# Performance work log

Hardware: AMD Instinct MI355X
Metric: run time of the kernel (lower is better)

The kernel has to match this reference:

```python
import jax, jax.numpy as jnp
import numpy as np

B, T, D = 4096, 64, 256       # expressions, max tokens per expression, encoding dim
N_SYM, N_OCC = 20000, 131072  # symbols, symbol occurrences


def setup_inputs() -> dict:
    key = jax.random.key(0)
    k1, k2, k3, k4, k5 = jax.random.split(key, 5)
    # unique flattened occurrence positions -> deterministic scatter
    rng = np.random.default_rng(0)
    flat_pos = rng.permutation(B * T)[:N_OCC].astype(np.int64)
    return {
        "expressions_encodings": jax.random.normal(k1, (B, T, D), dtype=jnp.float32),
        "symbols_encodings": jax.random.normal(k2, (N_SYM, D), dtype=jnp.float32),
        "Wf": jax.random.normal(k3, (D, 2 * D), dtype=jnp.float32) * 0.05,
        "bf": jnp.zeros((D,), dtype=jnp.float32),
        "Wa": jax.random.normal(k4, (D, 2 * D), dtype=jnp.float32) * 0.05,
        "ba": jnp.zeros((D,), dtype=jnp.float32),
        "expr_idx": jnp.asarray(flat_pos // T),
        "token_idx": jnp.asarray(flat_pos % T),
        "symbol_idx": jax.random.randint(k5, (N_OCC,), 0, N_SYM, dtype=jnp.int64),
    }


def reference(expressions_encodings, symbols_encodings, Wf, bf, Wa, ba,
              expr_idx, token_idx, symbol_idx):
    b, t, d = expressions_encodings.shape
    flat = expressions_encodings.reshape(b * t, d)            # [B*T, D]
    occ_pos = t * expr_idx + token_idx                        # [N_OCC]
    prev = flat[occ_pos]                                      # gather: [N_OCC, D]
    upd = symbols_encodings[symbol_idx]                       # gather: [N_OCC, D]
    concat = jnp.concatenate([prev, upd], axis=-1)            # [N_OCC, 2D]
    forget = jax.nn.sigmoid(concat @ Wf.T + bf)               # forget gate
    add = jax.nn.sigmoid(concat @ Wa.T + ba)                  # add gate
    new_occ = forget * prev + add * upd                       # gated update
    out = flat.at[occ_pos].set(new_occ)                       # scatter back
    return out.reshape(b, t, d)
```

## Files before the change

kernel.cpp:

```cpp
#include <hip/hip_runtime.h>

typedef __attribute__((ext_vector_type(8))) short short8;
typedef __attribute__((ext_vector_type(4))) short short4v;
typedef __attribute__((ext_vector_type(4))) float floatx4;

__device__ __forceinline__ unsigned short f2bf(float f) {
    unsigned int u = __float_as_uint(f);
    u += 0x7FFFu + ((u >> 16) & 1u);
    return (unsigned short)(u >> 16);
}
__device__ __forceinline__ float bf2f(unsigned short s) {
    return __uint_as_float(((unsigned int)s) << 16);
}
__device__ __forceinline__ float sigmoidf(float x) {
    return 1.f / (1.f + __expf(-x));
}

__global__ __launch_bounds__(256)
void convert_w_kernel(const float* __restrict__ Wf,
                      const float* __restrict__ Wa,
                      short* __restrict__ wswz)
{
    int id = blockIdx.x * 256 + threadIdx.x;
    int slot = id & 63;
    int ks   = (id >> 6) & 15;
    int g    = id >> 10;
    int l15  = slot & 15, lk = slot >> 4;
    const float* base = (g < 16) ? (Wf + (long)(g * 16 + l15) * 512)
                                 : (Wa + (long)((g - 16) * 16 + l15) * 512);
    const float* src = base + ks * 32 + lk * 8;
    floatx4 w0 = *(const floatx4*)src;
    floatx4 w1 = *(const floatx4*)(src + 4);
    short8 o;
    o[0] = (short)f2bf(w0[0]); o[1] = (short)f2bf(w0[1]);
    o[2] = (short)f2bf(w0[2]); o[3] = (short)f2bf(w0[3]);
    o[4] = (short)f2bf(w1[0]); o[5] = (short)f2bf(w1[1]);
    o[6] = (short)f2bf(w1[2]); o[7] = (short)f2bf(w1[3]);
    *(short8*)(wswz + (long)id * 8) = o;
}

__global__ __launch_bounds__(256)
void zero_flags_kernel(unsigned int* __restrict__ flags)
{
    flags[blockIdx.x * 256 + threadIdx.x] = 0u;
}

__global__ __launch_bounds__(256)
void mark_kernel(const int* __restrict__ ei, const int* __restrict__ ti,
                 unsigned char* __restrict__ flags, int n)
{
    int i = blockIdx.x * 256 + threadIdx.x;
    if (i < n) flags[64 * ei[i] + ti[i]] = 1;
}

__global__ __launch_bounds__(256)
void copy_rest_kernel(const float* __restrict__ flat,
                      const unsigned char* __restrict__ flags,
                      float* __restrict__ out, int nrows)
{
    const int lane = threadIdx.x & 63;
    const int w0   = (blockIdx.x * 256 + threadIdx.x) >> 6;
    const int nw   = (gridDim.x * 256) >> 6;
    for (int row = w0; row < nrows; row += nw) {
        if (flags[row]) continue;
        const floatx4* s = (const floatx4*)(flat + (long)row * 256);
        floatx4*       o = (floatx4*)(out + (long)row * 256);
        o[lane] = s[lane];
    }
}

__global__ __launch_bounds__(512, 4)
void gate_kernel(const float* __restrict__ flat,
                 const float* __restrict__ syms,
                 const float* __restrict__ bfb,
                 const float* __restrict__ bab,
                 const int* __restrict__ ei,
                 const int* __restrict__ ti,
                 const int* __restrict__ si,
                 const short* __restrict__ wswz,
                 float* __restrict__ out)
{
    __shared__ __align__(16) short A_lds[64 * 512];

    const int tid  = threadIdx.x;
    const int lane = tid & 63;
    const int w    = tid >> 6;
    const int occ0 = blockIdx.x * 64;

    int rowi[8];
    {
        int symi[8];
        #pragma unroll
        for (int i = 0; i < 8; ++i) {
            const int occ = occ0 + w * 8 + i;
            rowi[i] = 64 * ei[occ] + ti[occ];
            symi[i] = si[occ];
        }
        floatx4 va[8], vb[8];
        #pragma unroll
        for (int i = 0; i < 8; ++i) {
            const float* base = (lane < 32)
                ? (flat + (long)rowi[i] * 256 + lane * 8)
                : (syms + (long)symi[i] * 256 + (lane - 32) * 8);
            va[i] = *(const floatx4*)base;
            vb[i] = *(const floatx4*)(base + 4);
        }
        #pragma unroll
        for (int i = 0; i < 8; ++i) {
            short8 o;
            o[0] = (short)f2bf(va[i][0]); o[1] = (short)f2bf(va[i][1]);
            o[2] = (short)f2bf(va[i][2]); o[3] = (short)f2bf(va[i][3]);
            o[4] = (short)f2bf(vb[i][0]); o[5] = (short)f2bf(vb[i][1]);
            o[6] = (short)f2bf(vb[i][2]); o[7] = (short)f2bf(vb[i][3]);
            const int r = w * 8 + i;
            *(short8*)&A_lds[r * 512 + ((lane ^ (r & 7)) << 3)] = o;
        }
    }
    __syncthreads();

    const int l15 = lane & 15;
    const int lk  = lane >> 4;
    const short8* wsv = (const short8*)wswz;

    floatx4 acc[4][4];
    #pragma unroll
    for (int mi = 0; mi < 4; ++mi)
        #pragma unroll
        for (int c = 0; c < 4; ++c)
            acc[mi][c] = (floatx4){0.f, 0.f, 0.f, 0.f};

    #pragma unroll
    for (int ks = 0; ks < 16; ++ks) {
        short8 cb[4];
        #pragma unroll
        for (int mi = 0; mi < 4; ++mi) {
            const int m  = mi * 16 + l15;
            const int ch = (ks * 4 + lk) ^ (m & 7);
            cb[mi] = *(const short8*)&A_lds[m * 512 + (ch << 3)];
        }
        #pragma unroll
        for (int c = 0; c < 4; ++c) {
            const int g = (c < 2) ? (w * 2 + c) : (16 + w * 2 + (c - 2));
            const short8 wf = wsv[(g * 16 + ks) * 64 + lane];
            #pragma unroll
            for (int mi = 0; mi < 4; ++mi)
                acc[mi][c] = __builtin_amdgcn_mfma_f32_16x16x32_bf16(
                    wf, cb[mi], acc[mi][c], 0, 0, 0);
        }
    }
    __syncthreads();

    #pragma unroll
    for (int c = 0; c < 2; ++c) {
        const int d0 = w * 32 + c * 16 + lk * 4;
        const floatx4 bfv = *(const floatx4*)(bfb + d0);
        const floatx4 bav = *(const floatx4*)(bab + d0);
        #pragma unroll
        for (int mi = 0; mi < 4; ++mi) {
            const int m  = mi * 16 + l15;
            const int sw = m & 7;
            const int cp = (d0 >> 3) ^ sw;
            const int cu = (32 + (d0 >> 3)) ^ sw;
            const int sub = d0 & 7;
            short4v pv = *(const short4v*)&A_lds[m * 512 + (cp << 3) + sub];
            short4v uv = *(const short4v*)&A_lds[m * 512 + (cu << 3) + sub];
            short4v o;
            #pragma unroll
            for (int j = 0; j < 4; ++j) {
                float fg = sigmoidf(acc[mi][c][j]     + bfv[j]);
                float ag = sigmoidf(acc[mi][c + 2][j] + bav[j]);
                o[j] = (short)f2bf(fg * bf2f((unsigned short)pv[j])
                                 + ag * bf2f((unsigned short)uv[j]));
            }
            *(short4v*)&A_lds[m * 512 + (cp << 3) + sub] = o;
        }
    }
    __syncthreads();

    #pragma unroll
    for (int i = 0; i < 8; ++i) {
        const int r = w * 8 + i;
        short4v s = *(const short4v*)
            &A_lds[r * 512 + (((lane >> 1) ^ (r & 7)) << 3) + (lane & 1) * 4];
        floatx4 o4;
        o4[0] = bf2f((unsigned short)s[0]);
        o4[1] = bf2f((unsigned short)s[1]);
        o4[2] = bf2f((unsigned short)s[2]);
        o4[3] = bf2f((unsigned short)s[3]);
        *(floatx4*)(out + (long)rowi[i] * 256 + lane * 4) = o4;
    }
}

extern "C" void kernel_launch(void* const* d_in, const int* in_sizes, int n_in,
                              void* d_out, int out_size, void* d_ws, size_t ws_size,
                              hipStream_t stream) {
    const float* flat = (const float*)d_in[0];
    const float* syms = (const float*)d_in[1];
    const float* Wf   = (const float*)d_in[2];
    const float* bf   = (const float*)d_in[3];
    const float* Wa   = (const float*)d_in[4];
    const float* ba   = (const float*)d_in[5];
    const int* ei     = (const int*)d_in[6];
    const int* ti     = (const int*)d_in[7];
    const int* si     = (const int*)d_in[8];
    float* out        = (float*)d_out;

    short* wswz          = (short*)d_ws;
    unsigned char* flags = (unsigned char*)d_ws + 512 * 1024;

    const int n_occ = in_sizes[6];
    const int nrows = out_size / 256;

    zero_flags_kernel<<<nrows / 1024, 256, 0, stream>>>((unsigned int*)flags);
    mark_kernel<<<(n_occ + 255) / 256, 256, 0, stream>>>(ei, ti, flags, n_occ);
    convert_w_kernel<<<128, 256, 0, stream>>>(Wf, Wa, wswz);

    gate_kernel<<<n_occ / 64, 512, 0, stream>>>(flat, syms, bf, ba,
                                                ei, ti, si, wswz, out);

    copy_rest_kernel<<<2048, 256, 0, stream>>>(flat, flags, out, nrows);
}
```

Before: 231.8 us.

## Precompute per-symbol gate logits and software-pipeline occurrence gathers

```diff
diff --git a/kernel.cpp b/kernel.cpp
--- a/kernel.cpp
+++ b/kernel.cpp
@@ -3,6 +3,8 @@
 typedef __attribute__((ext_vector_type(8))) short short8;
 typedef __attribute__((ext_vector_type(4))) short short4v;
 typedef __attribute__((ext_vector_type(4))) float floatx4;
+
+#define NSYM 20000
 
 __device__ __forceinline__ unsigned short f2bf(float f) {
     unsigned int u = __float_as_uint(f);
@@ -15,20 +17,26 @@
 __device__ __forceinline__ float sigmoidf(float x) {
     return 1.f / (1.f + __expf(-x));
 }
+__device__ __forceinline__ short4v pack4(floatx4 v) {
+    short4v o;
+    o[0] = (short)f2bf(v[0]); o[1] = (short)f2bf(v[1]);
+    o[2] = (short)f2bf(v[2]); o[3] = (short)f2bf(v[3]);
+    return o;
+}
 
 __global__ __launch_bounds__(256)
 void convert_w_kernel(const float* __restrict__ Wf,
                       const float* __restrict__ Wa,
-                      short* __restrict__ wswz)
+                      short* __restrict__ wswzP,
+                      short* __restrict__ wswzU)
 {
     int id = blockIdx.x * 256 + threadIdx.x;
-    int slot = id & 63;
-    int ks   = (id >> 6) & 15;
-    int g    = id >> 10;
-    int l15  = slot & 15, lk = slot >> 4;
-    const float* base = (g < 16) ? (Wf + (long)(g * 16 + l15) * 512)
-                                 : (Wa + (long)((g - 16) * 16 + l15) * 512);
-    const float* src = base + ks * 32 + lk * 8;
+    int half = id >> 14;
+    int rem  = id & 16383;
+    int slot = rem & 63, ks = (rem >> 6) & 7, g = rem >> 9;
+    int l15 = slot & 15, lk = slot >> 4;
+    const float* wrow = ((g < 16) ? Wf : Wa) + (long)((g & 15) * 16 + l15) * 512;
+    const float* src  = wrow + half * 256 + ks * 32 + lk * 8;
     floatx4 w0 = *(const floatx4*)src;
     floatx4 w1 = *(const floatx4*)(src + 4);
     short8 o;
@@ -36,7 +44,8 @@
     o[2] = (short)f2bf(w0[2]); o[3] = (short)f2bf(w0[3]);
     o[4] = (short)f2bf(w1[0]); o[5] = (short)f2bf(w1[1]);
     o[6] = (short)f2bf(w1[2]); o[7] = (short)f2bf(w1[3]);
-    *(short8*)(wswz + (long)id * 8) = o;
+    short* dst = half ? wswzU : wswzP;
+    *(short8*)(dst + (long)((g * 8 + ks) * 64 + slot) * 8) = o;
 }
 
 __global__ __launch_bounds__(256)
@@ -70,124 +79,206 @@
 }
 
 __global__ __launch_bounds__(512, 4)
-void gate_kernel(const float* __restrict__ flat,
+void syms_logits_kernel(const float* __restrict__ syms,
+                        const float* __restrict__ bfb,
+                        const float* __restrict__ bab,
+                        const short* __restrict__ wswzU,
+                        short* __restrict__ symLg)
+{
+    __shared__ __align__(16) short S_lds[64 * 256];
+    const int tid = threadIdx.x;
+    const int r0  = blockIdx.x * 64;
+    {
+        const int r = tid >> 3, se = tid & 7;
+        const int s = min(r0 + r, NSYM - 1);
+        const float* srow = syms + (long)s * 256;
+        #pragma unroll
+        for (int i = 0; i < 8; ++i) {
+            const int gi = i * 8 + se;
+            floatx4 v = *(const floatx4*)(srow + gi * 4);
+            const int cb = gi >> 1, hf = gi & 1;
+            *(short4v*)&S_lds[r * 256 + ((cb ^ (r & 7)) << 3) + hf * 4] = pack4(v);
+        }
+    }
+    __syncthreads();
+
+    const int lane = tid & 63, w = tid >> 6, l15 = lane & 15, lk = lane >> 4;
+    floatx4 acc[4][4];
+    #pragma unroll
+    for (int mi = 0; mi < 4; ++mi)
+        #pragma unroll
+        for (int c = 0; c < 4; ++c)
+            acc[mi][c] = (floatx4){0.f, 0.f, 0.f, 0.f};
+
+    const short8* wsv = (const short8*)wswzU;
+    #pragma unroll
+    for (int ks = 0; ks < 8; ++ks) {
+        short8 cb[4];
+        #pragma unroll
+        for (int mi = 0; mi < 4; ++mi) {
+            const int m  = mi * 16 + l15;
+            const int ch = (ks * 4 + lk) ^ (m & 7);
+            cb[mi] = *(const short8*)&S_lds[m * 256 + (ch << 3)];
+        }
+        #pragma unroll
+        for (int c = 0; c < 4; ++c) {
+            const int g = (c < 2) ? (w * 2 + c) : (16 + w * 2 + (c - 2));
+            const short8 wf = wsv[(g * 8 + ks) * 64 + lane];
+            #pragma unroll
+            for (int mi = 0; mi < 4; ++mi)
+                acc[mi][c] = __builtin_amdgcn_mfma_f32_16x16x32_bf16(
+                    wf, cb[mi], acc[mi][c], 0, 0, 0);
+        }
+    }
+
+    #pragma unroll
+    for (int c = 0; c < 2; ++c) {
+        const int d0 = w * 32 + c * 16 + lk * 4;
+        const floatx4 bF = *(const floatx4*)(bfb + d0);
+        const floatx4 bA = *(const floatx4*)(bab + d0);
+        #pragma unroll
+        for (int mi = 0; mi < 4; ++mi) {
+            const int m = mi * 16 + l15;
+            const int s = r0 + m;
+            if (s < NSYM) {
+                short4v oF, oA;
+                #pragma unroll
+                for (int j = 0; j < 4; ++j) {
+                    oF[j] = (short)f2bf(acc[mi][c][j]     + bF[j]);
+                    oA[j] = (short)f2bf(acc[mi][c + 2][j] + bA[j]);
+                }
+                *(short4v*)(symLg + (long)s * 512 + d0)       = oF;
+                *(short4v*)(symLg + (long)s * 512 + 256 + d0) = oA;
+            }
+        }
+    }
+}
+
+__global__ __launch_bounds__(512, 4)
+void main_kernel(const float* __restrict__ flat,
                  const float* __restrict__ syms,
-                 const float* __restrict__ bfb,
-                 const float* __restrict__ bab,
                  const int* __restrict__ ei,
                  const int* __restrict__ ti,
                  const int* __restrict__ si,
-                 const short* __restrict__ wswz,
+                 const short* __restrict__ wswzP,
+                 const short* __restrict__ symLg,
                  float* __restrict__ out)
 {
-    __shared__ __align__(16) short A_lds[64 * 512];
+    __shared__ __align__(16) short L[32768];
 
     const int tid  = threadIdx.x;
-    const int lane = tid & 63;
-    const int w    = tid >> 6;
-    const int occ0 = blockIdx.x * 64;
-
-    int rowi[8];
-    {
-        int symi[8];
-        #pragma unroll
-        for (int i = 0; i < 8; ++i) {
-            const int occ = occ0 + w * 8 + i;
-            rowi[i] = 64 * ei[occ] + ti[occ];
-            symi[i] = si[occ];
-        }
-        floatx4 va[8], vb[8];
-        #pragma unroll
-        for (int i = 0; i < 8; ++i) {
-            const float* base = (lane < 32)
-                ? (flat + (long)rowi[i] * 256 + lane * 8)
-                : (syms + (long)symi[i] * 256 + (lane - 32) * 8);
-            va[i] = *(const floatx4*)base;
-            vb[i] = *(const floatx4*)(base + 4);
-        }
-        #pragma unroll
-        for (int i = 0; i < 8; ++i) {
-            short8 o;
-            o[0] = (short)f2bf(va[i][0]); o[1] = (short)f2bf(va[i][1]);
-            o[2] = (short)f2bf(va[i][2]); o[3] = (short)f2bf(va[i][3]);
-            o[4] = (short)f2bf(vb[i][0]); o[5] = (short)f2bf(vb[i][1]);
-            o[6] = (short)f2bf(vb[i][2]); o[7] = (short)f2bf(vb[i][3]);
-            const int r = w * 8 + i;
-            *(short8*)&A_lds[r * 512 + ((lane ^ (r & 7)) << 3)] = o;
-        }
-    }
-    __syncthreads();
-
-    const int l15 = lane & 15;
-    const int lk  = lane >> 4;
-    const short8* wsv = (const short8*)wswz;
-
-    floatx4 acc[4][4];
+    const int lane = tid & 63, w = tid >> 6, l15 = lane & 15, lk = lane >> 4;
+    const int r = tid >> 4, se = tid & 15;
+    const int base_occ = blockIdx.x * 256;
+
+    floatx4 pv[4], uv[4];
+    short8  sl[4];
+    auto issue = [&](int occ0) {
+        const int occ = occ0 + r;
+        const long rowp = 64 * ei[occ] + ti[occ];
+        const long syr  = si[occ];
+        const float* pr = flat + rowp * 256;
+        const float* ur = syms + syr * 256;
+        const short* lr = symLg + syr * 512;
+        #pragma unroll
+        for (int i = 0; i < 4; ++i) {
+            const int gi = i * 16 + se;
+            pv[i] = *(const floatx4*)(pr + gi * 4);
+            uv[i] = *(const floatx4*)(ur + gi * 4);
+            sl[i] = *(const short8*)(lr + gi * 8);
+        }
+    };
+
+    issue(base_occ);
+
+    const short8* wsv = (const short8*)wswzP;
+
     #pragma unroll
-    for (int mi = 0; mi < 4; ++mi)
-        #pragma unroll
-        for (int c = 0; c < 4; ++c)
-            acc[mi][c] = (floatx4){0.f, 0.f, 0.f, 0.f};
-
-    #pragma unroll
-    for (int ks = 0; ks < 16; ++ks) {
-        short8 cb[4];
-        #pragma unroll
-        for (int mi = 0; mi < 4; ++mi) {
-            const int m  = mi * 16 + l15;
-            const int ch = (ks * 4 + lk) ^ (m & 7);
-            cb[mi] = *(const short8*)&A_lds[m * 512 + (ch << 3)];
-        }
-        #pragma unroll
-        for (int c = 0; c < 4; ++c) {
-            const int g = (c < 2) ? (w * 2 + c) : (16 + w * 2 + (c - 2));
-            const short8 wf = wsv[(g * 16 + ks) * 64 + lane];
-            #pragma unroll
-            for (int mi = 0; mi < 4; ++mi)
-                acc[mi][c] = __builtin_amdgcn_mfma_f32_16x16x32_bf16(
-                    wf, cb[mi], acc[mi][c], 0, 0, 0);
-        }
-    }
-    __syncthreads();
-
-    #pragma unroll
-    for (int c = 0; c < 2; ++c) {
-        const int d0 = w * 32 + c * 16 + lk * 4;
-        const floatx4 bfv = *(const floatx4*)(bfb + d0);
-        const floatx4 bav = *(const floatx4*)(bab + d0);
-        #pragma unroll
-        for (int mi = 0; mi < 4; ++mi) {
-            const int m  = mi * 16 + l15;
-            const int sw = m & 7;
-            const int cp = (d0 >> 3) ^ sw;
-            const int cu = (32 + (d0 >> 3)) ^ sw;
-            const int sub = d0 & 7;
-            short4v pv = *(const short4v*)&A_lds[m * 512 + (cp << 3) + sub];
-            short4v uv = *(const short4v*)&A_lds[m * 512 + (cu << 3) + sub];
-            short4v o;
-            #pragma unroll
-            for (int j = 0; j < 4; ++j) {
-                float fg = sigmoidf(acc[mi][c][j]     + bfv[j]);
-                float ag = sigmoidf(acc[mi][c + 2][j] + bav[j]);
-                o[j] = (short)f2bf(fg * bf2f((unsigned short)pv[j])
-                                 + ag * bf2f((unsigned short)uv[j]));
+    for (int t = 0; t < 8; ++t) {
+        const int occ0 = base_occ + t * 32;
+        if (t) __syncthreads();
+        #pragma unroll
+        for (int i = 0; i < 4; ++i) {
+            const int gi = i * 16 + se;
+            const int cb = gi >> 1, hf = gi & 1;
+            const int so = ((cb ^ (r & 7)) << 3) + hf * 4;
+            *(short4v*)&L[r * 256 + so]        = pack4(pv[i]);
+            *(short4v*)&L[8192 + r * 256 + so] = pack4(uv[i]);
+            *(short8*)&L[16384 + r * 512 + ((gi ^ (r & 7)) << 3)] = sl[i];
+        }
+        __syncthreads();
+
+        if (t < 7) issue(occ0 + 32);
+
+        floatx4 acc[2][4];
+        #pragma unroll
+        for (int mi = 0; mi < 2; ++mi)
+            #pragma unroll
+            for (int c = 0; c < 4; ++c)
+                acc[mi][c] = (floatx4){0.f, 0.f, 0.f, 0.f};
+
+        #pragma unroll
+        for (int ks = 0; ks < 8; ++ks) {
+            short8 cb2[2];
+            #pragma unroll
+            for (int mi = 0; mi < 2; ++mi) {
+                const int m  = mi * 16 + l15;
+                const int ch = (ks * 4 + lk) ^ (m & 7);
+                cb2[mi] = *(const short8*)&L[m * 256 + (ch << 3)];
             }
-            *(short4v*)&A_lds[m * 512 + (cp << 3) + sub] = o;
-        }
-    }
-    __syncthreads();
-
-    #pragma unroll
-    for (int i = 0; i < 8; ++i) {
-        const int r = w * 8 + i;
-        short4v s = *(const short4v*)
-            &A_lds[r * 512 + (((lane >> 1) ^ (r & 7)) << 3) + (lane & 1) * 4];
-        floatx4 o4;
-        o4[0] = bf2f((unsigned short)s[0]);
-        o4[1] = bf2f((unsigned short)s[1]);
-        o4[2] = bf2f((unsigned short)s[2]);
-        o4[3] = bf2f((unsigned short)s[3]);
-        *(floatx4*)(out + (long)rowi[i] * 256 + lane * 4) = o4;
+            #pragma unroll
+            for (int c = 0; c < 4; ++c) {
+                const int g = (c < 2) ? (2 * w + c) : (16 + 2 * w + (c - 2));
+                const short8 wf = wsv[(g * 8 + ks) * 64 + lane];
+                acc[0][c] = __builtin_amdgcn_mfma_f32_16x16x32_bf16(
+                    wf, cb2[0], acc[0][c], 0, 0, 0);
+                acc[1][c] = __builtin_amdgcn_mfma_f32_16x16x32_bf16(
+                    wf, cb2[1], acc[1][c], 0, 0, 0);
+            }
+        }
+        __syncthreads();
+
+        #pragma unroll
+        for (int cc = 0; cc < 2; ++cc) {
+            const int d0  = (2 * w + cc) * 16 + lk * 4;
+            const int pch = d0 >> 3;
+            const int ps  = d0 & 7;
+            #pragma unroll
+            for (int mi = 0; mi < 2; ++mi) {
+                const int m = mi * 16 + l15, sw = m & 7;
+                const int slot = ((pch ^ sw) << 3) + ps;
+                short4v pvv = *(const short4v*)&L[m * 256 + slot];
+                short4v uvv = *(const short4v*)&L[8192 + m * 256 + slot];
+                short4v sF  = *(const short4v*)&L[16384 + m * 512 + slot];
+                short4v sA  = *(const short4v*)&L[16384 + m * 512 +
+                                                  (((32 + pch) ^ sw) << 3) + ps];
+                short4v o;
+                #pragma unroll
+                for (int j = 0; j < 4; ++j) {
+                    float fg = sigmoidf(acc[mi][cc][j]     + bf2f((unsigned short)sF[j]));
+                    float ag = sigmoidf(acc[mi][2 + cc][j] + bf2f((unsigned short)sA[j]));
+                    o[j] = (short)f2bf(fg * bf2f((unsigned short)pvv[j])
+                                     + ag * bf2f((unsigned short)uvv[j]));
+                }
+                *(short4v*)&L[m * 256 + slot] = o;
+            }
+        }
+        __syncthreads();
+
+        #pragma unroll
+        for (int i = 0; i < 4; ++i) {
+            const int rr  = w * 4 + i;
+            const int occ = occ0 + rr;
+            const long orow = 64 * ei[occ] + ti[occ];
+            short4v sv = *(const short4v*)
+                &L[rr * 256 + (((lane >> 1) ^ (rr & 7)) << 3) + (lane & 1) * 4];
+            floatx4 o4;
+            o4[0] = bf2f((unsigned short)sv[0]);
+            o4[1] = bf2f((unsigned short)sv[1]);
+            o4[2] = bf2f((unsigned short)sv[2]);
+            o4[3] = bf2f((unsigned short)sv[3]);
+            *(floatx4*)(out + orow * 256 + lane * 4) = o4;
+        }
     }
 }
 
@@ -205,18 +296,22 @@
     const int* si     = (const int*)d_in[8];
     float* out        = (float*)d_out;
 
-    short* wswz          = (short*)d_ws;
-    unsigned char* flags = (unsigned char*)d_ws + 512 * 1024;
+    short* wswzP         = (short*)d_ws;
+    short* wswzU         = (short*)d_ws + 131072;
+    unsigned char* flags = (unsigned char*)d_ws + 524288;
+    short* symLg         = (short*)((char*)d_ws + 786432);
 
     const int n_occ = in_sizes[6];
     const int nrows = out_size / 256;
 
     zero_flags_kernel<<<nrows / 1024, 256, 0, stream>>>((unsigned int*)flags);
     mark_kernel<<<(n_occ + 255) / 256, 256, 0, stream>>>(ei, ti, flags, n_occ);
-    convert_w_kernel<<<128, 256, 0, stream>>>(Wf, Wa, wswz);
-
-    gate_kernel<<<n_occ / 64, 512, 0, stream>>>(flat, syms, bf, ba,
-                                                ei, ti, si, wswz, out);
+    convert_w_kernel<<<128, 256, 0, stream>>>(Wf, Wa, wswzP, wswzU);
+    syms_logits_kernel<<<(NSYM + 63) / 64, 512, 0, stream>>>(syms, bf, ba,
+                                                             wswzU, symLg);
+
+    main_kernel<<<n_occ / 256, 512, 0, stream>>>(flat, syms, ei, ti, si,
+                                                 wswzP, symLg, out);
 
     copy_rest_kernel<<<2048, 256, 0, stream>>>(flat, flags, out, nrows);
 }
```

Result: slower. 295.1 us (+27.3%).

## Stream all rows in dense tiles with inverse symbol map instead of gather+copy

Applied to the files above, without the earlier changes.

```diff
diff --git a/kernel.cpp b/kernel.cpp
--- a/kernel.cpp
+++ b/kernel.cpp
@@ -2,6 +2,7 @@
 
 typedef __attribute__((ext_vector_type(8))) short short8;
 typedef __attribute__((ext_vector_type(4))) short short4v;
+typedef __attribute__((ext_vector_type(2))) unsigned int uint2v;
 typedef __attribute__((ext_vector_type(4))) float floatx4;
 
 __device__ __forceinline__ unsigned short f2bf(float f) {
@@ -14,6 +15,13 @@
 }
 __device__ __forceinline__ float sigmoidf(float x) {
     return 1.f / (1.f + __expf(-x));
+}
+__device__ __forceinline__ short4v pack4(floatx4 v) {
+    unsigned int a, b;
+    asm("v_cvt_pk_bf16_f32 %0, %1, %2" : "=v"(a) : "v"(v[0]), "v"(v[1]));
+    asm("v_cvt_pk_bf16_f32 %0, %1, %2" : "=v"(b) : "v"(v[2]), "v"(v[3]));
+    uint2v u; u[0] = a; u[1] = b;
+    return __builtin_bit_cast(short4v, u);
 }
 
 __global__ __launch_bounds__(256)
@@ -40,154 +48,165 @@
 }
 
 __global__ __launch_bounds__(256)
-void zero_flags_kernel(unsigned int* __restrict__ flags)
-{
-    flags[blockIdx.x * 256 + threadIdx.x] = 0u;
+void zero_inv_kernel(int* __restrict__ inv)
+{
+    inv[blockIdx.x * 256 + threadIdx.x] = 0;
 }
 
 __global__ __launch_bounds__(256)
-void mark_kernel(const int* __restrict__ ei, const int* __restrict__ ti,
-                 unsigned char* __restrict__ flags, int n)
+void scatter_inv_kernel(const int* __restrict__ ei, const int* __restrict__ ti,
+                        const int* __restrict__ si, int* __restrict__ inv, int n)
 {
     int i = blockIdx.x * 256 + threadIdx.x;
-    if (i < n) flags[64 * ei[i] + ti[i]] = 1;
-}
-
-__global__ __launch_bounds__(256)
-void copy_rest_kernel(const float* __restrict__ flat,
-                      const unsigned char* __restrict__ flags,
-                      float* __restrict__ out, int nrows)
-{
-    const int lane = threadIdx.x & 63;
-    const int w0   = (blockIdx.x * 256 + threadIdx.x) >> 6;
-    const int nw   = (gridDim.x * 256) >> 6;
-    for (int row = w0; row < nrows; row += nw) {
-        if (flags[row]) continue;
-        const floatx4* s = (const floatx4*)(flat + (long)row * 256);
-        floatx4*       o = (floatx4*)(out + (long)row * 256);
-        o[lane] = s[lane];
-    }
+    if (i < n) inv[64 * ei[i] + ti[i]] = si[i] + 1;
 }
 
 __global__ __launch_bounds__(512, 4)
-void gate_kernel(const float* __restrict__ flat,
-                 const float* __restrict__ syms,
-                 const float* __restrict__ bfb,
-                 const float* __restrict__ bab,
-                 const int* __restrict__ ei,
-                 const int* __restrict__ ti,
-                 const int* __restrict__ si,
-                 const short* __restrict__ wswz,
-                 float* __restrict__ out)
-{
-    __shared__ __align__(16) short A_lds[64 * 512];
+void stream_kernel(const float* __restrict__ flat,
+                   const float* __restrict__ syms,
+                   const float* __restrict__ bfb,
+                   const float* __restrict__ bab,
+                   const int* __restrict__ inv,
+                   const short* __restrict__ wswz,
+                   float* __restrict__ out, int tiles_per_block)
+{
+    __shared__ __align__(16) short P[64 * 256];
+    __shared__ __align__(16) short U[64 * 256];
+    __shared__ int flg[64];
 
     const int tid  = threadIdx.x;
-    const int lane = tid & 63;
-    const int w    = tid >> 6;
-    const int occ0 = blockIdx.x * 64;
-
-    int rowi[8];
-    {
-        int symi[8];
+    const int lane = tid & 63, w = tid >> 6, l15 = lane & 15, lk = lane >> 4;
+    const int tt0  = blockIdx.x * tiles_per_block;
+
+    floatx4 pv[8];
+    auto issueP = [&](int tile) {
+        const float* src = flat + (long)tile * 16384 + tid * 4;
+        #pragma unroll
+        for (int i = 0; i < 8; ++i) pv[i] = *(const floatx4*)(src + i * 2048);
+    };
+    issueP(tt0);
+
+    const short8* wsv = (const short8*)wswz;
+
+    for (int t = 0; t < tiles_per_block; ++t) {
+        const int tile = tt0 + t;
+        const int row0 = tile * 64;
+        if (t) __syncthreads();
+
+        if (tid < 64) flg[tid] = inv[row0 + tid];
+
+        const int r16 = tid >> 4, se = tid & 15;
+        const int symA = inv[row0 + r16];
+        const int symB = inv[row0 + 32 + r16];
+        floatx4 uva[4], uvb[4];
+        if (symA > 0) {
+            const float* ur = syms + (long)(symA - 1) * 256;
+            #pragma unroll
+            for (int i = 0; i < 4; ++i)
+                uva[i] = *(const floatx4*)(ur + (i * 16 + se) * 4);
+        }
+        if (symB > 0) {
+            const float* ur = syms + (long)(symB - 1) * 256;
+            #pragma unroll
+            for (int i = 0; i < 4; ++i)
+                uvb[i] = *(const floatx4*)(ur + (i * 16 + se) * 4);
+        }
+
         #pragma unroll
         for (int i = 0; i < 8; ++i) {
-            const int occ = occ0 + w * 8 + i;
-            rowi[i] = 64 * ei[occ] + ti[occ];
-            symi[i] = si[occ];
-        }
-        floatx4 va[8], vb[8];
+            const int f  = tid + i * 512;
+            const int rr = f >> 6;
+            const int gi = f & 63;
+            const int cb = gi >> 1, hf = gi & 1;
+            *(short4v*)&P[rr * 256 + ((cb ^ (rr & 7)) << 3) + hf * 4] = pack4(pv[i]);
+        }
+        if (symA > 0) {
+            #pragma unroll
+            for (int i = 0; i < 4; ++i) {
+                const int gi = i * 16 + se, cb = gi >> 1, hf = gi & 1;
+                *(short4v*)&U[r16 * 256 + ((cb ^ (r16 & 7)) << 3) + hf * 4] = pack4(uva[i]);
+            }
+        }
+        if (symB > 0) {
+            const int rr = 32 + r16;
+            #pragma unroll
+            for (int i = 0; i < 4; ++i) {
+                const int gi = i * 16 + se, cb = gi >> 1, hf = gi & 1;
+                *(short4v*)&U[rr * 256 + ((cb ^ (rr & 7)) << 3) + hf * 4] = pack4(uvb[i]);
+            }
+        }
+        __syncthreads();
+
+        if (t + 1 < tiles_per_block) issueP(tile + 1);
+
+        floatx4 acc[4][4];
+        #pragma unroll
+        for (int mi = 0; mi < 4; ++mi)
+            #pragma unroll
+            for (int c = 0; c < 4; ++c)
+                acc[mi][c] = (floatx4){0.f, 0.f, 0.f, 0.f};
+
+        #pragma unroll
+        for (int ks = 0; ks < 16; ++ks) {
+            short8 cb2[4];
+            #pragma unroll
+            for (int mi = 0; mi < 4; ++mi) {
+                const int m = mi * 16 + l15;
+                cb2[mi] = (ks < 8)
+                    ? *(const short8*)&P[m * 256 + (((ks * 4 + lk) ^ (m & 7)) << 3)]
+                    : *(const short8*)&U[m * 256 + ((((ks - 8) * 4 + lk) ^ (m & 7)) << 3)];
+            }
+            #pragma unroll
+            for (int c = 0; c < 4; ++c) {
+                const int g = (c < 2) ? (w * 2 + c) : (16 + w * 2 + (c - 2));
+                const short8 wf = wsv[(g * 16 + ks) * 64 + lane];
+                #pragma unroll
+                for (int mi = 0; mi < 4; ++mi)
+                    acc[mi][c] = __builtin_amdgcn_mfma_f32_16x16x32_bf16(
+                        wf, cb2[mi], acc[mi][c], 0, 0, 0);
+            }
+        }
+        __syncthreads();
+
+        #pragma unroll
+        for (int c = 0; c < 2; ++c) {
+            const int d0 = w * 32 + c * 16 + lk * 4;
+            const floatx4 bfv = *(const floatx4*)(bfb + d0);
+            const floatx4 bav = *(const floatx4*)(bab + d0);
+            #pragma unroll
+            for (int mi = 0; mi < 4; ++mi) {
+                const int m = mi * 16 + l15;
+                if (flg[m] > 0) {
+                    const int sw = m & 7;
+                    const int slot = (((d0 >> 3) ^ sw) << 3) + (d0 & 7);
+                    short4v pvv = *(const short4v*)&P[m * 256 + slot];
+                    short4v uvv = *(const short4v*)&U[m * 256 + slot];
+                    floatx4 res;
+                    #pragma unroll
+                    for (int j = 0; j < 4; ++j) {
+                        float fg = sigmoidf(acc[mi][c][j]     + bfv[j]);
+                        float ag = sigmoidf(acc[mi][c + 2][j] + bav[j]);
+                        res[j] = fg * bf2f((unsigned short)pvv[j])
+                               + ag * bf2f((unsigned short)uvv[j]);
+                    }
+                    *(short4v*)&P[m * 256 + slot] = pack4(res);
+                }
+            }
+        }
+        __syncthreads();
+
         #pragma unroll
         for (int i = 0; i < 8; ++i) {
-            const float* base = (lane < 32)
-                ? (flat + (long)rowi[i] * 256 + lane * 8)
-                : (syms + (long)symi[i] * 256 + (lane - 32) * 8);
-            va[i] = *(const floatx4*)base;
-            vb[i] = *(const floatx4*)(base + 4);
-        }
-        #pragma unroll
-        for (int i = 0; i < 8; ++i) {
-            short8 o;
-            o[0] = (short)f2bf(va[i][0]); o[1] = (short)f2bf(va[i][1]);
-            o[2] = (short)f2bf(va[i][2]); o[3] = (short)f2bf(va[i][3]);
-            o[4] = (short)f2bf(vb[i][0]); o[5] = (short)f2bf(vb[i][1]);
-            o[6] = (short)f2bf(vb[i][2]); o[7] = (short)f2bf(vb[i][3]);
-            const int r = w * 8 + i;
-            *(short8*)&A_lds[r * 512 + ((lane ^ (r & 7)) << 3)] = o;
-        }
-    }
-    __syncthreads();
-
-    const int l15 = lane & 15;
-    const int lk  = lane >> 4;
-    const short8* wsv = (const short8*)wswz;
-
-    floatx4 acc[4][4];
-    #pragma unroll
-    for (int mi = 0; mi < 4; ++mi)
-        #pragma unroll
-        for (int c = 0; c < 4; ++c)
-            acc[mi][c] = (floatx4){0.f, 0.f, 0.f, 0.f};
-
-    #pragma unroll
-    for (int ks = 0; ks < 16; ++ks) {
-        short8 cb[4];
-        #pragma unroll
-        for (int mi = 0; mi < 4; ++mi) {
-            const int m  = mi * 16 + l15;
-            const int ch = (ks * 4 + lk) ^ (m & 7);
-            cb[mi] = *(const short8*)&A_lds[m * 512 + (ch << 3)];
-        }
-        #pragma unroll
-        for (int c = 0; c < 4; ++c) {
-            const int g = (c < 2) ? (w * 2 + c) : (16 + w * 2 + (c - 2));
-            const short8 wf = wsv[(g * 16 + ks) * 64 + lane];
-            #pragma unroll
-            for (int mi = 0; mi < 4; ++mi)
-                acc[mi][c] = __builtin_amdgcn_mfma_f32_16x16x32_bf16(
-                    wf, cb[mi], acc[mi][c], 0, 0, 0);
-        }
-    }
-    __syncthreads();
-
-    #pragma unroll
-    for (int c = 0; c < 2; ++c) {
-        const int d0 = w * 32 + c * 16 + lk * 4;
-        const floatx4 bfv = *(const floatx4*)(bfb + d0);
-        const floatx4 bav = *(const floatx4*)(bab + d0);
-        #pragma unroll
-        for (int mi = 0; mi < 4; ++mi) {
-            const int m  = mi * 16 + l15;
-            const int sw = m & 7;
-            const int cp = (d0 >> 3) ^ sw;
-            const int cu = (32 + (d0 >> 3)) ^ sw;
-            const int sub = d0 & 7;
-            short4v pv = *(const short4v*)&A_lds[m * 512 + (cp << 3) + sub];
-            short4v uv = *(const short4v*)&A_lds[m * 512 + (cu << 3) + sub];
-            short4v o;
-            #pragma unroll
-            for (int j = 0; j < 4; ++j) {
-                float fg = sigmoidf(acc[mi][c][j]     + bfv[j]);
-                float ag = sigmoidf(acc[mi][c + 2][j] + bav[j]);
-                o[j] = (short)f2bf(fg * bf2f((unsigned short)pv[j])
-                                 + ag * bf2f((unsigned short)uv[j]));
-            }
-            *(short4v*)&A_lds[m * 512 + (cp << 3) + sub] = o;
-        }
-    }
-    __syncthreads();
-
-    #pragma unroll
-    for (int i = 0; i < 8; ++i) {
-        const int r = w * 8 + i;
-        short4v s = *(const short4v*)
-            &A_lds[r * 512 + (((lane >> 1) ^ (r & 7)) << 3) + (lane & 1) * 4];
-        floatx4 o4;
-        o4[0] = bf2f((unsigned short)s[0]);
-        o4[1] = bf2f((unsigned short)s[1]);
-        o4[2] = bf2f((unsigned short)s[2]);
-        o4[3] = bf2f((unsigned short)s[3]);
-        *(floatx4*)(out + (long)rowi[i] * 256 + lane * 4) = o4;
+            const int rr = w * 8 + i;
+            short4v s = *(const short4v*)
+                &P[rr * 256 + (((lane >> 1) ^ (rr & 7)) << 3) + (lane & 1) * 4];
+            floatx4 o4;
+            o4[0] = bf2f((unsigned short)s[0]);
+            o4[1] = bf2f((unsigned short)s[1]);
+            o4[2] = bf2f((unsigned short)s[2]);
+            o4[3] = bf2f((unsigned short)s[3]);
+            *(floatx4*)(out + (long)(row0 + rr) * 256 + lane * 4) = o4;
+        }
     }
 }
 
@@ -205,18 +224,20 @@
     const int* si     = (const int*)d_in[8];
     float* out        = (float*)d_out;
 
-    short* wswz          = (short*)d_ws;
-    unsigned char* flags = (unsigned char*)d_ws + 512 * 1024;
+    short* wswz = (short*)d_ws;
+    int*   inv  = (int*)((char*)d_ws + 512 * 1024);
 
     const int n_occ = in_sizes[6];
     const int nrows = out_size / 256;
 
-    zero_flags_kernel<<<nrows / 1024, 256, 0, stream>>>((unsigned int*)flags);
-    mark_kernel<<<(n_occ + 255) / 256, 256, 0, stream>>>(ei, ti, flags, n_occ);
+    zero_inv_kernel<<<nrows / 256, 256, 0, stream>>>(inv);
+    scatter_inv_kernel<<<(n_occ + 255) / 256, 256, 0, stream>>>(ei, ti, si,
+                                                                inv, n_occ);
     convert_w_kernel<<<128, 256, 0, stream>>>(Wf, Wa, wswz);
 
-    gate_kernel<<<n_occ / 64, 512, 0, stream>>>(flat, syms, bf, ba,
-                                                ei, ti, si, wswz, out);
-
-    copy_rest_kernel<<<2048, 256, 0, stream>>>(flat, flags, out, nrows);
-}
+    const int ntiles = nrows / 64;
+    const int nblk   = 512;
+    const int tpb    = ntiles / nblk;
+    stream_kernel<<<nblk, 512, 0, stream>>>(flat, syms, bf, ba, inv, wswz,
+                                            out, tpb);
+}
```

Measured after the change: 806.7 us. 248% more time.

## Split gate GEMM into symbol and prev halves to overlap gather latency

Applied to the files above, without the earlier changes.

```diff
diff --git a/kernel.cpp b/kernel.cpp
--- a/kernel.cpp
+++ b/kernel.cpp
@@ -2,6 +2,7 @@
 
 typedef __attribute__((ext_vector_type(8))) short short8;
 typedef __attribute__((ext_vector_type(4))) short short4v;
+typedef __attribute__((ext_vector_type(2))) unsigned int uint2v;
 typedef __attribute__((ext_vector_type(4))) float floatx4;
 
 __device__ __forceinline__ unsigned short f2bf(float f) {
@@ -14,6 +15,13 @@
 }
 __device__ __forceinline__ float sigmoidf(float x) {
     return 1.f / (1.f + __expf(-x));
+}
+__device__ __forceinline__ short4v pack4(floatx4 v) {
+    unsigned int a, b;
+    asm("v_cvt_pk_bf16_f32 %0, %1, %2" : "=v"(a) : "v"(v[0]), "v"(v[1]));
+    asm("v_cvt_pk_bf16_f32 %0, %1, %2" : "=v"(b) : "v"(v[2]), "v"(v[3]));
+    uint2v u; u[0] = a; u[1] = b;
+    return __builtin_bit_cast(short4v, u);
 }
 
 __global__ __launch_bounds__(256)
@@ -80,47 +88,40 @@
                  const short* __restrict__ wswz,
                  float* __restrict__ out)
 {
-    __shared__ __align__(16) short A_lds[64 * 512];
+    __shared__ __align__(16) short P[64 * 256];
+    __shared__ __align__(16) short U[64 * 256];
 
     const int tid  = threadIdx.x;
     const int lane = tid & 63;
     const int w    = tid >> 6;
     const int occ0 = blockIdx.x * 64;
-
-    int rowi[8];
-    {
-        int symi[8];
-        #pragma unroll
-        for (int i = 0; i < 8; ++i) {
-            const int occ = occ0 + w * 8 + i;
-            rowi[i] = 64 * ei[occ] + ti[occ];
-            symi[i] = si[occ];
-        }
-        floatx4 va[8], vb[8];
-        #pragma unroll
-        for (int i = 0; i < 8; ++i) {
-            const float* base = (lane < 32)
-                ? (flat + (long)rowi[i] * 256 + lane * 8)
-                : (syms + (long)symi[i] * 256 + (lane - 32) * 8);
-            va[i] = *(const floatx4*)base;
-            vb[i] = *(const floatx4*)(base + 4);
-        }
-        #pragma unroll
-        for (int i = 0; i < 8; ++i) {
-            short8 o;
-            o[0] = (short)f2bf(va[i][0]); o[1] = (short)f2bf(va[i][1]);
-            o[2] = (short)f2bf(va[i][2]); o[3] = (short)f2bf(va[i][3]);
-            o[4] = (short)f2bf(vb[i][0]); o[5] = (short)f2bf(vb[i][1]);
-            o[6] = (short)f2bf(vb[i][2]); o[7] = (short)f2bf(vb[i][3]);
-            const int r = w * 8 + i;
-            *(short8*)&A_lds[r * 512 + ((lane ^ (r & 7)) << 3)] = o;
-        }
-    }
-    __syncthreads();
-
-    const int l15 = lane & 15;
-    const int lk  = lane >> 4;
-    const short8* wsv = (const short8*)wswz;
+    const int l15  = lane & 15;
+    const int lk   = lane >> 4;
+
+    int rowi[8], symi[8];
+    #pragma unroll
+    for (int i = 0; i < 8; ++i) {
+        const int occ = occ0 + w * 8 + i;
+        rowi[i] = 64 * ei[occ] + ti[occ];
+        symi[i] = si[occ];
+    }
+
+    floatx4 uv[8];
+    #pragma unroll
+    for (int i = 0; i < 8; ++i)
+        uv[i] = *(const floatx4*)(syms + (long)symi[i] * 256 + lane * 4);
+    floatx4 pv[8];
+    #pragma unroll
+    for (int i = 0; i < 8; ++i)
+        pv[i] = *(const floatx4*)(flat + (long)rowi[i] * 256 + lane * 4);
+
+    const int cb = lane >> 1, hf = lane & 1;
+    #pragma unroll
+    for (int i = 0; i < 8; ++i) {
+        const int r = w * 8 + i;
+        *(short4v*)&U[r * 256 + ((cb ^ (r & 7)) << 3) + hf * 4] = pack4(uv[i]);
+    }
+    __syncthreads();
 
     floatx4 acc[4][4];
     #pragma unroll
@@ -129,14 +130,46 @@
         for (int c = 0; c < 4; ++c)
             acc[mi][c] = (floatx4){0.f, 0.f, 0.f, 0.f};
 
-    #pragma unroll
-    for (int ks = 0; ks < 16; ++ks) {
-        short8 cb[4];
+    const short8* wsv = (const short8*)wswz;
+
+    __builtin_amdgcn_s_setprio(1);
+    #pragma unroll
+    for (int ks = 0; ks < 8; ++ks) {
+        short8 cb2[4];
         #pragma unroll
         for (int mi = 0; mi < 4; ++mi) {
             const int m  = mi * 16 + l15;
             const int ch = (ks * 4 + lk) ^ (m & 7);
-            cb[mi] = *(const short8*)&A_lds[m * 512 + (ch << 3)];
+            cb2[mi] = *(const short8*)&U[m * 256 + (ch << 3)];
+        }
+        #pragma unroll
+        for (int c = 0; c < 4; ++c) {
+            const int g = (c < 2) ? (w * 2 + c) : (16 + w * 2 + (c - 2));
+            const short8 wf = wsv[(g * 16 + 8 + ks) * 64 + lane];
+            #pragma unroll
+            for (int mi = 0; mi < 4; ++mi)
+                acc[mi][c] = __builtin_amdgcn_mfma_f32_16x16x32_bf16(
+                    wf, cb2[mi], acc[mi][c], 0, 0, 0);
+        }
+    }
+    __builtin_amdgcn_s_setprio(0);
+
+    #pragma unroll
+    for (int i = 0; i < 8; ++i) {
+        const int r = w * 8 + i;
+        *(short4v*)&P[r * 256 + ((cb ^ (r & 7)) << 3) + hf * 4] = pack4(pv[i]);
+    }
+    __syncthreads();
+
+    __builtin_amdgcn_s_setprio(1);
+    #pragma unroll
+    for (int ks = 0; ks < 8; ++ks) {
+        short8 cb2[4];
+        #pragma unroll
+        for (int mi = 0; mi < 4; ++mi) {
+            const int m  = mi * 16 + l15;
+            const int ch = (ks * 4 + lk) ^ (m & 7);
+            cb2[mi] = *(const short8*)&P[m * 256 + (ch << 3)];
         }
         #pragma unroll
         for (int c = 0; c < 4; ++c) {
@@ -145,9 +178,10 @@
             #pragma unroll
             for (int mi = 0; mi < 4; ++mi)
                 acc[mi][c] = __builtin_amdgcn_mfma_f32_16x16x32_bf16(
-                    wf, cb[mi], acc[mi][c], 0, 0, 0);
-        }
-    }
+                    wf, cb2[mi], acc[mi][c], 0, 0, 0);
+        }
+    }
+    __builtin_amdgcn_s_setprio(0);
     __syncthreads();
 
     #pragma unroll
@@ -159,29 +193,27 @@
         for (int mi = 0; mi < 4; ++mi) {
             const int m  = mi * 16 + l15;
             const int sw = m & 7;
-            const int cp = (d0 >> 3) ^ sw;
-            const int cu = (32 + (d0 >> 3)) ^ sw;
-            const int sub = d0 & 7;
-            short4v pv = *(const short4v*)&A_lds[m * 512 + (cp << 3) + sub];
-            short4v uv = *(const short4v*)&A_lds[m * 512 + (cu << 3) + sub];
-            short4v o;
+            const int slot = (((d0 >> 3) ^ sw) << 3) + (d0 & 7);
+            short4v pvv = *(const short4v*)&P[m * 256 + slot];
+            short4v uvv = *(const short4v*)&U[m * 256 + slot];
+            floatx4 res;
             #pragma unroll
             for (int j = 0; j < 4; ++j) {
                 float fg = sigmoidf(acc[mi][c][j]     + bfv[j]);
                 float ag = sigmoidf(acc[mi][c + 2][j] + bav[j]);
-                o[j] = (short)f2bf(fg * bf2f((unsigned short)pv[j])
-                                 + ag * bf2f((unsigned short)uv[j]));
+                res[j] = fg * bf2f((unsigned short)pvv[j])
+                       + ag * bf2f((unsigned short)uvv[j]);
             }
-            *(short4v*)&A_lds[m * 512 + (cp << 3) + sub] = o;
-        }
-    }
-    __syncthreads();
-
-    #pragma unroll
-    for (int i = 0; i < 8; ++i) {
-        const int r = w * 8 + i;
+            *(short4v*)&P[m * 256 + slot] = pack4(res);
+        }
+    }
+    __syncthreads();
+
+    #pragma unroll
+    for (int i = 0; i < 8; ++i) {
+        const int rr = w * 8 + i;
         short4v s = *(const short4v*)
-            &A_lds[r * 512 + (((lane >> 1) ^ (r & 7)) << 3) + (lane & 1) * 4];
+            &P[rr * 256 + (((lane >> 1) ^ (rr & 7)) << 3) + (lane & 1) * 4];
         floatx4 o4;
         o4[0] = bf2f((unsigned short)s[0]);
         o4[1] = bf2f((unsigned short)s[1]);
```

Result: slower. 352.5 us (+52.1%).
